# Performance work log

Hardware: AMD Instinct MI355X
Metric: run time of the kernel (lower is better)

Reference implementation:

```python
import jax, jax.numpy as jnp
import numpy as np

B, C, N = 16, 1024, 32
H, Dh = 8, 16          # num_head, dim per head
D = H * Dh             # 128, model feature dim
SCALE = 0.5


def setup_inputs() -> dict:
    key = jax.random.key(0)
    ks = jax.random.split(key, 12)
    inp = {
        "atom_query": jax.random.normal(ks[0], (B, C, D), jnp.float32),
        "atom_neighbor": jax.random.normal(ks[1], (B, C, N, D), jnp.float32),
        "local_distance": jax.random.uniform(ks[2], (B, C, N, 1), jnp.float32),
        "mask": jnp.ones((B, C, N), jnp.float32),
        # Dense params (kernel [in, out], bias [out]) as in keras Dense
        "Wq": jax.random.normal(ks[3], (D, D), jnp.float32) / np.sqrt(D),
        "bq": jnp.zeros((D,), jnp.float32),
        "Wk": jax.random.normal(ks[4], (D, D), jnp.float32) / np.sqrt(D),
        "bk": jnp.zeros((D,), jnp.float32),
        "Wv": jax.random.normal(ks[5], (D, D), jnp.float32) / np.sqrt(D),
        "bv": jnp.zeros((D,), jnp.float32),
        "Wf": jax.random.normal(ks[6], (1, D), jnp.float32),
        "bf": jnp.zeros((D,), jnp.float32),
    }
    return inp


def reference(atom_query, atom_neighbor, local_distance, mask,
              Wq, bq, Wk, bk, Wv, bv, Wf, bf):
    # distance filter with swish activation: x * sigmoid(x)
    ld = local_distance @ Wf + bf              # [B,C,N,D]
    ld = ld * jax.nn.sigmoid(ld)
    an = atom_neighbor * ld                    # distance-gated neighbors

    query = atom_query @ Wq + bq               # [B,C,D]
    k = (an @ Wk + bk).reshape(B, C, N, H, Dh)  # [B,C,N,H,d]
    v = (an @ Wv + bv).reshape(B, C, N, H, Dh)

    q = query.reshape(B, C, H, Dh) * (float(Dh) ** (-SCALE))
    energy = jnp.einsum('bchd,bcnhd->bhcn', q, k)           # [B,H,C,N]
    energy = energy + (1.0 - mask[:, None, :, :]) * (-1e9)
    attn = jax.nn.softmax(energy, axis=-1)

    ctx = jnp.einsum('bhcn,bcnhd->bcnhd', attn, v)          # per-neighbor context
    ctx = ctx * mask[:, :, :, None, None]
    ctx = ctx.reshape(B, C, N, H * Dh)
    context = jnp.sum(ctx, axis=2) + query                  # [B,C,D]
    return attn, context
```

## Files before the change

kernel.cpp:

```cpp
#include <hip/hip_runtime.h>
#include <hip/hip_fp16.h>
#include <cstdint>


#define B_ 16
#define C_ 1024
#define N_ 32
#define H_ 8
#define D_ 128
#define G_ 4
#define T_ 256

typedef unsigned short u16;
typedef unsigned int u32;
typedef __fp16 hw2 __attribute__((ext_vector_type(2)));

__device__ __forceinline__ u32 pkrtz(float a, float b) {
    hw2 r = __builtin_amdgcn_cvt_pkrtz(a, b);
    return __builtin_bit_cast(u32, r);
}
__device__ __forceinline__ float fdot2(u32 a, u32 b, float c) {
#if __has_builtin(__builtin_amdgcn_fdot2)
    return __builtin_amdgcn_fdot2(__builtin_bit_cast(hw2, a),
                                  __builtin_bit_cast(hw2, b), c, false);
#else
    float2 A = __half22float2(__builtin_bit_cast(__half2, a));
    float2 B = __half22float2(__builtin_bit_cast(__half2, b));
    return fmaf(A.y, B.y, fmaf(A.x, B.x, c));
#endif
}
__device__ __forceinline__ __half2 fma2(u32 a, u32 b, __half2 c) {
    return __hfma2(__builtin_bit_cast(__half2, a),
                   __builtin_bit_cast(__half2, b), c);
}
__device__ __forceinline__ float swishf(float x) {
    float s = __builtin_amdgcn_rcpf(1.0f + __expf(-x));
    return x * s;
}

__global__ __launch_bounds__(T_, 2)
void la_kernel(const float* __restrict__ aq_g,  const float* __restrict__ an_g,
               const float* __restrict__ dist_g, const float* __restrict__ mask_g,
               const float* __restrict__ wq_g,  const float* __restrict__ bq_g,
               const float* __restrict__ wk_g,
               const float* __restrict__ wv_g,  const float* __restrict__ bv_g,
               const float* __restrict__ wf_g,  const float* __restrict__ bfb_g,
               float* __restrict__ attn_o, float* __restrict__ ctx_o)
{
    __shared__ __align__(16) u16   s_an[G_ * N_ * 136];
    __shared__ __align__(16) float s_ts[G_ * H_ * 132];
    __shared__ float s_q[G_][D_];
    __shared__ float s_aq[G_][D_];
    __shared__ __align__(8) float s_eat[G_][H_][33];
    __shared__ float s_dist[G_][N_];
    __shared__ float s_mask[G_][N_];
    __shared__ float s_asum[G_][H_];
    __shared__ __align__(16) float s_wf[D_];
    __shared__ __align__(16) float s_bfb[D_];

    const int tid = threadIdx.x;
    const int b   = blockIdx.x >> 8;
    const int c0  = (blockIdx.x & 255) << 2;

    const int op = tid & 63;
    const int js = tid >> 6;

    float2 wq2[32];
    #pragma unroll
    for (int i = 0; i < 32; i++)
        wq2[i] = ((const float2*)(wq_g + (size_t)(js * 32 + i) * D_))[op];

    if (tid < D_) {
        s_wf[tid]  = wf_g[tid];
        s_bfb[tid] = bfb_g[tid];
        int c = tid >> 5, n = tid & 31;
        int gi = (b * C_ + c0 + c) * N_ + n;
        s_dist[c][n] = dist_g[gi];
        s_mask[c][n] = mask_g[gi];
    }
    {
        int c = tid >> 7, d = tid & 127;
        s_aq[c][d] = aq_g[(b * C_ + c0 + c) * D_ + d];
        int i2 = tid + 256;
        c = i2 >> 7; d = i2 & 127;
        s_aq[c][d] = aq_g[(b * C_ + c0 + c) * D_ + d];
    }
    __syncthreads();

    {
        const float4* gan = (const float4*)(an_g + (size_t)(b * C_ + c0) * N_ * D_);
        #pragma unroll
        for (int k = 0; k < 16; k++) {
            int ci = k * T_ + tid;
            float4 v = gan[ci];
            int d4 = ci & 31, n = (ci >> 5) & 31, c = ci >> 10;
            float dist = s_dist[c][n];
            int d0 = d4 << 2;
            float4 wf = *(const float4*)&s_wf[d0];
            float4 bb = *(const float4*)&s_bfb[d0];
            float g0 = swishf(fmaf(dist, wf.x, bb.x));
            float g1 = swishf(fmaf(dist, wf.y, bb.y));
            float g2 = swishf(fmaf(dist, wf.z, bb.z));
            float g3 = swishf(fmaf(dist, wf.w, bb.w));
            u32 o0 = pkrtz(v.x * g0, v.y * g1);
            u32 o1 = pkrtz(v.z * g2, v.w * g3);
            *(uint2*)(s_an + (c * N_ + n) * 136 + d0) = make_uint2(o0, o1);
        }
    }

    {
        float acc0[G_], acc1[G_];
        #pragma unroll
        for (int c = 0; c < G_; c++) { acc0[c] = 0.f; acc1[c] = 0.f; }
        #pragma unroll
        for (int i4 = 0; i4 < 8; i4++) {
            #pragma unroll
            for (int c = 0; c < G_; c++) {
                float4 a4 = *(const float4*)&s_aq[c][js * 32 + i4 * 4];
                float2 w0 = wq2[i4 * 4], w1 = wq2[i4 * 4 + 1];
                float2 w2 = wq2[i4 * 4 + 2], w3 = wq2[i4 * 4 + 3];
                acc0[c] = fmaf(a4.x, w0.x, acc0[c]); acc1[c] = fmaf(a4.x, w0.y, acc1[c]);
                acc0[c] = fmaf(a4.y, w1.x, acc0[c]); acc1[c] = fmaf(a4.y, w1.y, acc1[c]);
                acc0[c] = fmaf(a4.z, w2.x, acc0[c]); acc1[c] = fmaf(a4.z, w2.y, acc1[c]);
                acc0[c] = fmaf(a4.w, w3.x, acc0[c]); acc1[c] = fmaf(a4.w, w3.y, acc1[c]);
            }
        }
        float* s_part = s_ts;
        #pragma unroll
        for (int c = 0; c < G_; c++) {
            *(float2*)&s_part[(js * G_ + c) * D_ + 2 * op] = make_float2(acc0[c], acc1[c]);
        }
    }
    __syncthreads();

    {
        const float* s_part = s_ts;
        #pragma unroll
        for (int r = 0; r < 2; r++) {
            int lin = r * 256 + tid;
            int c = lin >> 7, od = lin & 127;
            float sum = s_part[(0 * G_ + c) * D_ + od] + s_part[(1 * G_ + c) * D_ + od]
                      + s_part[(2 * G_ + c) * D_ + od] + s_part[(3 * G_ + c) * D_ + od];
            s_q[c][od] = sum + bq_g[od];
        }
    }
    __syncthreads();

    float2 wv2[32];
    #pragma unroll
    for (int i = 0; i < 32; i++)
        wv2[i] = ((const float2*)(wv_g + (size_t)(js * 32 + i) * D_))[op];

    {
        u32* t32 = (u32*)s_ts;
        int h = tid & 7, jb = tid >> 3;
        float wk[4][16];
        #pragma unroll
        for (int jj = 0; jj < 4; jj++) {
            int j = 2 * jb + (jj & 1) + (jj >> 1) * 64;
            const float4* pk = (const float4*)(wk_g + j * D_ + h * 16);
            float4 k0 = pk[0], k1 = pk[1], k2 = pk[2], k3 = pk[3];
            wk[jj][0]  = k0.x; wk[jj][1]  = k0.y; wk[jj][2]  = k0.z; wk[jj][3]  = k0.w;
            wk[jj][4]  = k1.x; wk[jj][5]  = k1.y; wk[jj][6]  = k1.z; wk[jj][7]  = k1.w;
            wk[jj][8]  = k2.x; wk[jj][9]  = k2.y; wk[jj][10] = k2.z; wk[jj][11] = k2.w;
            wk[jj][12] = k3.x; wk[jj][13] = k3.y; wk[jj][14] = k3.z; wk[jj][15] = k3.w;
        }
        #pragma unroll
        for (int c = 0; c < G_; c++) {
            float qv[16];
            #pragma unroll
            for (int d = 0; d < 16; d++) qv[d] = s_q[c][h * 16 + d];
            float acc[4];
            #pragma unroll
            for (int jj = 0; jj < 4; jj++) {
                float a = 0.f;
                #pragma unroll
                for (int d = 0; d < 16; d++) a = fmaf(qv[d], wk[jj][d], a);
                acc[jj] = a * 0.25f;
            }
            t32[(c * 8 + h) * 68 + jb]      = pkrtz(acc[0], acc[1]);
            t32[(c * 8 + h) * 68 + 32 + jb] = pkrtz(acc[2], acc[3]);
        }
    }
    __syncthreads();

    {
        const u32* t32 = (const u32*)s_ts;
        int c = tid >> 6, h = (tid >> 3) & 7, n0 = tid & 7;
        const uint4* trow = (const uint4*)(t32 + (c * 8 + h) * 68);
        float acc[4] = {0.f, 0.f, 0.f, 0.f};
        #pragma unroll
        for (int jc = 0; jc < 16; jc++) {
            uint4 t4 = trow[jc];
            #pragma unroll
            for (int r = 0; r < 4; r++) {
                int n = n0 + r * 8;
                uint4 a4 = *(const uint4*)(s_an + (c * N_ + n) * 136 + jc * 8);
                float s = acc[r];
                s = fdot2(a4.x, t4.x, s);
                s = fdot2(a4.y, t4.y, s);
                s = fdot2(a4.z, t4.z, s);
                s = fdot2(a4.w, t4.w, s);
                acc[r] = s;
            }
        }
        #pragma unroll
        for (int r = 0; r < 4; r++) {
            int n = n0 + r * 8;
            float mk = s_mask[c][n];
            s_eat[c][h][n] = acc[r] + (1.0f - mk) * (-1.0e9f);
        }
    }
    __syncthreads();

    if (tid < G_ * H_) {
        int c = tid >> 3, h = tid & 7;
        float e[N_];
        float m = -3.0e38f;
        #pragma unroll
        for (int n = 0; n < N_; n++) { e[n] = s_eat[c][h][n]; m = fmaxf(m, e[n]); }
        float sum = 0.f;
        #pragma unroll
        for (int n = 0; n < N_; n++) { float p = __expf(e[n] - m); e[n] = p; sum += p; }
        float inv = 1.0f / sum;
        u32* ampk = (u32*)&s_eat[c][h][0];
        float asum = 0.f;
        size_t off = ((size_t)(b * H_ + h) * C_ + (c0 + c)) * N_;
        #pragma unroll
        for (int n4 = 0; n4 < 8; n4++) {
            float4 w;
            w.x = e[n4 * 4]     * inv;
            w.y = e[n4 * 4 + 1] * inv;
            w.z = e[n4 * 4 + 2] * inv;
            w.w = e[n4 * 4 + 3] * inv;
            *(float4*)(attn_o + off + n4 * 4) = w;
            float am0 = w.x * s_mask[c][n4 * 4];
            float am1 = w.y * s_mask[c][n4 * 4 + 1];
            float am2 = w.z * s_mask[c][n4 * 4 + 2];
            float am3 = w.w * s_mask[c][n4 * 4 + 3];
            asum += am0 + am1 + am2 + am3;
            ampk[n4 * 4]     = pkrtz(am0, am0);
            ampk[n4 * 4 + 1] = pkrtz(am1, am1);
            ampk[n4 * 4 + 2] = pkrtz(am2, am2);
            ampk[n4 * 4 + 3] = pkrtz(am3, am3);
        }
        s_asum[c][h] = asum;
    }
    __syncthreads();

    {
        int c = tid >> 6, h = (tid >> 3) & 7, jg = tid & 7;
        const u32* ampk = (const u32*)&s_eat[c][h][0];
        __half2 acc2[8];
        #pragma unroll
        for (int i = 0; i < 8; i++) acc2[i] = __float2half2_rn(0.f);
        #pragma unroll 4
        for (int n = 0; n < N_; n++) {
            u32 am2 = ampk[n];
            const uint4* arow = (const uint4*)(s_an + (c * N_ + n) * 136 + jg * 16);
            uint4 a0 = arow[0], a1 = arow[1];
            acc2[0] = fma2(a0.x, am2, acc2[0]);
            acc2[1] = fma2(a0.y, am2, acc2[1]);
            acc2[2] = fma2(a0.z, am2, acc2[2]);
            acc2[3] = fma2(a0.w, am2, acc2[3]);
            acc2[4] = fma2(a1.x, am2, acc2[4]);
            acc2[5] = fma2(a1.y, am2, acc2[5]);
            acc2[6] = fma2(a1.z, am2, acc2[6]);
            acc2[7] = fma2(a1.w, am2, acc2[7]);
        }
        float* srow = &s_ts[(c * H_ + h) * 132 + jg * 16];
        #pragma unroll
        for (int p = 0; p < 4; p++) {
            float2 lo = __half22float2(acc2[p * 2]);
            float2 hi = __half22float2(acc2[p * 2 + 1]);
            *(float4*)(srow + p * 4) = make_float4(lo.x, lo.y, hi.x, hi.y);
        }
    }
    __syncthreads();

    {
        int h = op >> 3;
        float acc0[G_], acc1[G_];
        #pragma unroll
        for (int c = 0; c < G_; c++) { acc0[c] = 0.f; acc1[c] = 0.f; }
        #pragma unroll
        for (int i4 = 0; i4 < 8; i4++) {
            #pragma unroll
            for (int c = 0; c < G_; c++) {
                float4 s4 = *(const float4*)&s_ts[(c * H_ + h) * 132 + js * 32 + i4 * 4];
                float2 w0 = wv2[i4 * 4], w1 = wv2[i4 * 4 + 1];
                float2 w2 = wv2[i4 * 4 + 2], w3 = wv2[i4 * 4 + 3];
                acc0[c] = fmaf(s4.x, w0.x, acc0[c]); acc1[c] = fmaf(s4.x, w0.y, acc1[c]);
                acc0[c] = fmaf(s4.y, w1.x, acc0[c]); acc1[c] = fmaf(s4.y, w1.y, acc1[c]);
                acc0[c] = fmaf(s4.z, w2.x, acc0[c]); acc1[c] = fmaf(s4.z, w2.y, acc1[c]);
                acc0[c] = fmaf(s4.w, w3.x, acc0[c]); acc1[c] = fmaf(s4.w, w3.y, acc1[c]);
            }
        }
        float* s_gp = (float*)s_an;
        #pragma unroll
        for (int c = 0; c < G_; c++) {
            *(float2*)&s_gp[(js * G_ + c) * D_ + 2 * op] = make_float2(acc0[c], acc1[c]);
        }
    }
    __syncthreads();

    {
        const float* s_gp = (const float*)s_an;
        #pragma unroll
        for (int r = 0; r < 2; r++) {
            int lin = r * 256 + tid;
            int c = lin >> 7, od = lin & 127;
            int h = od >> 4;
            float sum = s_gp[(0 * G_ + c) * D_ + od] + s_gp[(1 * G_ + c) * D_ + od]
                      + s_gp[(2 * G_ + c) * D_ + od] + s_gp[(3 * G_ + c) * D_ + od];
            float r0 = sum + s_asum[c][h] * bv_g[od] + s_q[c][od];
            ctx_o[((size_t)(b * C_ + c0 + c)) * D_ + od] = r0;
        }
    }
}

extern "C" void kernel_launch(void* const* d_in, const int* in_sizes, int n_in,
                              void* d_out, int out_size, void* d_ws, size_t ws_size,
                              hipStream_t stream) {
    const float* aq   = (const float*)d_in[0];
    const float* an   = (const float*)d_in[1];
    const float* dist = (const float*)d_in[2];
    const float* mask = (const float*)d_in[3];
    const float* wq   = (const float*)d_in[4];
    const float* bq   = (const float*)d_in[5];
    const float* wk   = (const float*)d_in[6];
    const float* wv   = (const float*)d_in[8];
    const float* bv   = (const float*)d_in[9];
    const float* wf   = (const float*)d_in[10];
    const float* bfb  = (const float*)d_in[11];

    float* attn_o = (float*)d_out;
    float* ctx_o  = attn_o + (size_t)B_ * H_ * C_ * N_;

    dim3 grid(B_ * C_ / G_), block(T_);
    hipLaunchKernelGGL(la_kernel, grid, block, 0, stream,
                       aq, an, dist, mask, wq, bq, wk, wv, bv, wf, bfb,
                       attn_o, ctx_o);
}
```

Baseline: 437.4 us.

## Shrink LDS footprint via buffer aliasing to fit three blocks per CU

Shared-memory use is cut so that three 256-thread blocks can be resident per CU, and the launch bound is raised from 2 to 3 blocks. The attention-score scratch buffer shrinks to a packed half2 layout. The query input staging is aliased onto s_eat. The per-head context scratch is moved into the no-longer-needed s_an region, and the Wv partial sums go to s_ts. The query buffer is padded to 20 floats per head so the Wk stage can use float4 loads with fewer bank conflicts. The higher occupancy target tightens the per-thread register budget, which could cause spills given the large register arrays for wq, wv and wk.

```diff
diff --git a/kernel.cpp b/kernel.cpp
--- a/kernel.cpp
+++ b/kernel.cpp
@@ -38,7 +38,7 @@
     return x * s;
 }
 
-__global__ __launch_bounds__(T_, 2)
+__global__ __launch_bounds__(T_, 3)
 void la_kernel(const float* __restrict__ aq_g,  const float* __restrict__ an_g,
                const float* __restrict__ dist_g, const float* __restrict__ mask_g,
                const float* __restrict__ wq_g,  const float* __restrict__ bq_g,
@@ -48,10 +48,9 @@
                float* __restrict__ attn_o, float* __restrict__ ctx_o)
 {
     __shared__ __align__(16) u16   s_an[G_ * N_ * 136];
-    __shared__ __align__(16) float s_ts[G_ * H_ * 132];
-    __shared__ float s_q[G_][D_];
-    __shared__ float s_aq[G_][D_];
-    __shared__ __align__(8) float s_eat[G_][H_][33];
+    __shared__ __align__(16) u32   s_ts[G_ * H_ * 68];
+    __shared__ __align__(16) float s_q[G_][H_ * 20];
+    __shared__ __align__(16) float s_eat[G_][H_][33];
     __shared__ float s_dist[G_][N_];
     __shared__ float s_mask[G_][N_];
     __shared__ float s_asum[G_][H_];
@@ -70,6 +69,7 @@
     for (int i = 0; i < 32; i++)
         wq2[i] = ((const float2*)(wq_g + (size_t)(js * 32 + i) * D_))[op];
 
+    float* s_aqf = (float*)s_eat;
     if (tid < D_) {
         s_wf[tid]  = wf_g[tid];
         s_bfb[tid] = bfb_g[tid];
@@ -79,11 +79,9 @@
         s_mask[c][n] = mask_g[gi];
     }
     {
-        int c = tid >> 7, d = tid & 127;
-        s_aq[c][d] = aq_g[(b * C_ + c0 + c) * D_ + d];
+        s_aqf[tid] = aq_g[(b * C_ + c0 + (tid >> 7)) * D_ + (tid & 127)];
         int i2 = tid + 256;
-        c = i2 >> 7; d = i2 & 127;
-        s_aq[c][d] = aq_g[(b * C_ + c0 + c) * D_ + d];
+        s_aqf[i2] = aq_g[(b * C_ + c0 + (i2 >> 7)) * D_ + (i2 & 127)];
     }
     __syncthreads();
 
@@ -116,7 +114,7 @@
         for (int i4 = 0; i4 < 8; i4++) {
             #pragma unroll
             for (int c = 0; c < G_; c++) {
-                float4 a4 = *(const float4*)&s_aq[c][js * 32 + i4 * 4];
+                float4 a4 = *(const float4*)&s_aqf[c * D_ + js * 32 + i4 * 4];
                 float2 w0 = wq2[i4 * 4], w1 = wq2[i4 * 4 + 1];
                 float2 w2 = wq2[i4 * 4 + 2], w3 = wq2[i4 * 4 + 3];
                 acc0[c] = fmaf(a4.x, w0.x, acc0[c]); acc1[c] = fmaf(a4.x, w0.y, acc1[c]);
@@ -125,7 +123,7 @@
                 acc0[c] = fmaf(a4.w, w3.x, acc0[c]); acc1[c] = fmaf(a4.w, w3.y, acc1[c]);
             }
         }
-        float* s_part = s_ts;
+        float* s_part = (float*)s_ts;
         #pragma unroll
         for (int c = 0; c < G_; c++) {
             *(float2*)&s_part[(js * G_ + c) * D_ + 2 * op] = make_float2(acc0[c], acc1[c]);
@@ -134,14 +132,14 @@
     __syncthreads();
 
     {
-        const float* s_part = s_ts;
+        const float* s_part = (const float*)s_ts;
         #pragma unroll
         for (int r = 0; r < 2; r++) {
             int lin = r * 256 + tid;
             int c = lin >> 7, od = lin & 127;
             float sum = s_part[(0 * G_ + c) * D_ + od] + s_part[(1 * G_ + c) * D_ + od]
                       + s_part[(2 * G_ + c) * D_ + od] + s_part[(3 * G_ + c) * D_ + od];
-            s_q[c][od] = sum + bq_g[od];
+            s_q[c][(od >> 4) * 20 + (od & 15)] = sum + bq_g[od];
         }
     }
     __syncthreads();
@@ -152,7 +150,7 @@
         wv2[i] = ((const float2*)(wv_g + (size_t)(js * 32 + i) * D_))[op];
 
     {
-        u32* t32 = (u32*)s_ts;
+        u32* t32 = s_ts;
         int h = tid & 7, jb = tid >> 3;
         float wk[4][16];
         #pragma unroll
@@ -167,9 +165,10 @@
         }
         #pragma unroll
         for (int c = 0; c < G_; c++) {
-            float qv[16];
-            #pragma unroll
-            for (int d = 0; d < 16; d++) qv[d] = s_q[c][h * 16 + d];
+            const float4* pq = (const float4*)&s_q[c][h * 20];
+            float4 q0 = pq[0], q1 = pq[1], q2 = pq[2], q3 = pq[3];
+            float qv[16] = { q0.x, q0.y, q0.z, q0.w, q1.x, q1.y, q1.z, q1.w,
+                             q2.x, q2.y, q2.z, q2.w, q3.x, q3.y, q3.z, q3.w };
             float acc[4];
             #pragma unroll
             for (int jj = 0; jj < 4; jj++) {
@@ -185,7 +184,7 @@
     __syncthreads();
 
     {
-        const u32* t32 = (const u32*)s_ts;
+        const u32* t32 = s_ts;
         int c = tid >> 6, h = (tid >> 3) & 7, n0 = tid & 7;
         const uint4* trow = (const uint4*)(t32 + (c * 8 + h) * 68);
         float acc[4] = {0.f, 0.f, 0.f, 0.f};
@@ -268,7 +267,7 @@
             acc2[6] = fma2(a1.z, am2, acc2[6]);
             acc2[7] = fma2(a1.w, am2, acc2[7]);
         }
-        float* srow = &s_ts[(c * H_ + h) * 132 + jg * 16];
+        float* srow = (float*)(s_an + c * (N_ * 136)) + h * 132 + jg * 16;
         #pragma unroll
         for (int p = 0; p < 4; p++) {
             float2 lo = __half22float2(acc2[p * 2]);
@@ -287,7 +286,8 @@
         for (int i4 = 0; i4 < 8; i4++) {
             #pragma unroll
             for (int c = 0; c < G_; c++) {
-                float4 s4 = *(const float4*)&s_ts[(c * H_ + h) * 132 + js * 32 + i4 * 4];
+                const float* sc_ = (const float*)(s_an + c * (N_ * 136));
+                float4 s4 = *(const float4*)&sc_[h * 132 + js * 32 + i4 * 4];
                 float2 w0 = wv2[i4 * 4], w1 = wv2[i4 * 4 + 1];
                 float2 w2 = wv2[i4 * 4 + 2], w3 = wv2[i4 * 4 + 3];
                 acc0[c] = fmaf(s4.x, w0.x, acc0[c]); acc1[c] = fmaf(s4.x, w0.y, acc1[c]);
@@ -296,7 +296,7 @@
                 acc0[c] = fmaf(s4.w, w3.x, acc0[c]); acc1[c] = fmaf(s4.w, w3.y, acc1[c]);
             }
         }
-        float* s_gp = (float*)s_an;
+        float* s_gp = (float*)s_ts;
         #pragma unroll
         for (int c = 0; c < G_; c++) {
             *(float2*)&s_gp[(js * G_ + c) * D_ + 2 * op] = make_float2(acc0[c], acc1[c]);
@@ -305,7 +305,7 @@
     __syncthreads();
 
     {
-        const float* s_gp = (const float*)s_an;
+        const float* s_gp = (const float*)s_ts;
         #pragma unroll
         for (int r = 0; r < 2; r++) {
             int lin = r * 256 + tid;
@@ -313,7 +313,7 @@
             int h = od >> 4;
             float sum = s_gp[(0 * G_ + c) * D_ + od] + s_gp[(1 * G_ + c) * D_ + od]
                       + s_gp[(2 * G_ + c) * D_ + od] + s_gp[(3 * G_ + c) * D_ + od];
-            float r0 = sum + s_asum[c][h] * bv_g[od] + s_q[c][od];
+            float r0 = sum + s_asum[c][h] * bv_g[od] + s_q[c][h * 20 + (od & 15)];
             ctx_o[((size_t)(b * C_ + c0 + c)) * D_ + od] = r0;
         }
     }
```

After: 453.5 us. 1.04x slower.
